# Performance work log

Measured on AMD Instinct MI355X. Metric: run time of the kernel, lower is better.

Reference implementation:

```python
import jax, jax.numpy as jnp
import numpy as np

NEG_SLOPE = 0.01  # torch nn.LeakyReLU default


def setup_inputs() -> dict:
    key = jax.random.key(0)
    k1, k2, k3, k4 = jax.random.split(key, 4)
    B, N, d = 256, 64, 64
    embeddings = jax.random.normal(k1, (B, N, d), dtype=jnp.float32)
    # nn.Linear(em_dim, em_dim): weight [d, d] (out, in), bias [d]
    w_W = jax.random.normal(k2, (d, d), dtype=jnp.float32) / np.sqrt(d)
    w_b = jax.random.normal(k3, (d,), dtype=jnp.float32) * 0.01
    # nn.Linear(em_dim, 1): weight [1, d] -> stored as [d], bias [1]
    a_W = jax.random.normal(k4, (d,), dtype=jnp.float32) / np.sqrt(d)
    a_b = jnp.zeros((1,), dtype=jnp.float32)
    return {"embeddings": embeddings, "w_W": w_W, "w_b": w_b, "a_W": a_W, "a_b": a_b}


def reference(embeddings, w_W, w_b, a_W, a_b):
    # pairwise elementwise product: value[b,i,j,d] = emb[b,i,d] * emb[b,j,d]
    value = embeddings[:, :, None, :] * embeddings[:, None, :, :]  # [B,N,N,d]
    # small linear d->d (torch Linear: x @ W.T + b)
    qk = jnp.einsum('bijd,ed->bije', value, w_W) + w_b
    qk = jnp.where(qk >= 0, qk, NEG_SLOPE * qk)  # LeakyReLU
    # dropout is identity in eval mode
    logits = jnp.einsum('bijd,d->bij', qk, a_W) + a_b[0]  # linear d->1, squeeze
    alphas = jax.nn.softmax(logits, axis=-1)[..., None]  # [B,N,N,1]
    return alphas, value
```

## Files before the change

kernel.cpp:

```cpp
#include <hip/hip_runtime.h>

typedef __attribute__((ext_vector_type(8))) short short8;
typedef __attribute__((ext_vector_type(4))) float floatx4;
typedef __attribute__((ext_vector_type(4))) int   intx4;

#define NEG_SLOPE 0.01f

__device__ __forceinline__ short f2bf(float f) {
    unsigned u = __float_as_uint(f);
    unsigned r = (u + 0x7FFFu + ((u >> 16) & 1u)) >> 16;
    return (short)r;
}

__device__ __forceinline__ int pack2(float x, float y) {
    return (int)(unsigned short)f2bf(x) | ((int)(unsigned short)f2bf(y) << 16);
}

__global__ __launch_bounds__(256, 4)
void afm_kernel(const float* __restrict__ emb,
                const float* __restrict__ wW,
                const float* __restrict__ wb,
                const float* __restrict__ aW,
                float* __restrict__ aOut,
                float* __restrict__ vOut) {
    __shared__ __align__(16) char smem[29184];

    const int tid = threadIdx.x;
    const int blk = blockIdx.x;
    const int g   = blk >> 1;
    const int b   = g >> 4;
    const int iq  = g & 15;

    const float* embB = emb + (size_t)b * 4096;

    if ((blk & 1) == 0) {
        float (*sE)[64] = (float (*)[64])smem;
        #pragma unroll
        for (int k = 0; k < 4; ++k) {
            int f4 = k * 256 + tid;
            float4 x = *(const float4*)(embB + (f4 << 2));
            *(float4*)&sE[0][f4 << 2] = x;
        }
        __syncthreads();

        const int d0 = (tid & 15) << 2;
        const int jb = tid >> 4;
        floatx4 ei[4];
        #pragma unroll
        for (int il = 0; il < 4; ++il)
            ei[il] = *(floatx4*)&sE[iq * 4 + il][d0];

        #pragma unroll
        for (int c = 0; c < 16; ++c) {
            const int il = c >> 2;
            const int j  = ((c & 3) << 4) + jb;
            floatx4 ej = *(floatx4*)&sE[j][d0];
            floatx4 x  = ei[il] * ej;
            float* dst = vOut + ((size_t)(b * 64 + iq * 4 + il) << 12)
                              + ((c & 3) << 10) + (tid << 2);
            __builtin_nontemporal_store(x, (floatx4*)dst);
        }
        return;
    }

    float (*sW)[68]   = (float (*)[68])smem;
    short (*sEb)[72]  = (short (*)[72])(smem + 17408);
    float (*sei)[64]  = (float (*)[64])(smem + 26624);
    float *swb        = (float *)(smem + 27648);
    float *saw        = (float *)(smem + 27904);
    float (*slog)[64] = (float (*)[64])(smem + 28160);

    const int lane = tid & 63;
    const int w    = tid >> 6;
    const int i    = iq * 4 + w;

    {
        int row = tid >> 2;
        int c0  = (tid & 3) << 4;
        const float* src = embB + row * 64 + c0;
        float4 a0 = *(const float4*)(src);
        float4 a1 = *(const float4*)(src + 4);
        float4 a2 = *(const float4*)(src + 8);
        float4 a3 = *(const float4*)(src + 12);
        intx4 q0, q1;
        q0[0] = pack2(a0.x, a0.y); q0[1] = pack2(a0.z, a0.w);
        q0[2] = pack2(a1.x, a1.y); q0[3] = pack2(a1.z, a1.w);
        q1[0] = pack2(a2.x, a2.y); q1[1] = pack2(a2.z, a2.w);
        q1[2] = pack2(a3.x, a3.y); q1[3] = pack2(a3.z, a3.w);
        *(intx4*)&sEb[row][c0]     = q0;
        *(intx4*)&sEb[row][c0 + 8] = q1;

        const float* wsrc = wW + row * 64 + c0;
        float4 b0 = *(const float4*)(wsrc);
        float4 b1 = *(const float4*)(wsrc + 4);
        float4 b2 = *(const float4*)(wsrc + 8);
        float4 b3 = *(const float4*)(wsrc + 12);
        *(float4*)&sW[row][c0]      = b0;
        *(float4*)&sW[row][c0 + 4]  = b1;
        *(float4*)&sW[row][c0 + 8]  = b2;
        *(float4*)&sW[row][c0 + 12] = b3;

        sei[w][lane] = embB[i * 64 + lane];
        if (tid < 64)        swb[tid]       = wb[tid];
        else if (tid < 128)  saw[tid - 64]  = aW[tid - 64];
    }
    __syncthreads();

    const int lo = lane & 15, hi = lane >> 4;

    short8 bf[2][4];
    #pragma unroll
    for (int kt = 0; kt < 2; ++kt) {
        const int d0 = kt * 32 + hi * 8;
        float4 ei0 = *(float4*)&sei[w][d0];
        float4 ei1 = *(float4*)&sei[w][d0 + 4];
        #pragma unroll
        for (int et = 0; et < 4; ++et) {
            int e = et * 16 + lo;
            float4 w0 = *(float4*)&sW[e][d0];
            float4 w1 = *(float4*)&sW[e][d0 + 4];
            short8 t;
            t[0] = f2bf(w0.x * ei0.x); t[1] = f2bf(w0.y * ei0.y);
            t[2] = f2bf(w0.z * ei0.z); t[3] = f2bf(w0.w * ei0.w);
            t[4] = f2bf(w1.x * ei1.x); t[5] = f2bf(w1.y * ei1.y);
            t[6] = f2bf(w1.z * ei1.z); t[7] = f2bf(w1.w * ei1.w);
            bf[kt][et] = t;
        }
    }

    float wbv[4], awv[4];
    #pragma unroll
    for (int et = 0; et < 4; ++et) {
        int e = et * 16 + lo;
        wbv[et] = swb[e];
        awv[et] = saw[e];
    }

    float lg[16];
    #pragma unroll
    for (int jt = 0; jt < 4; ++jt) {
        floatx4 acc[4];
        #pragma unroll
        for (int et = 0; et < 4; ++et)
            acc[et] = (floatx4){0.f, 0.f, 0.f, 0.f};
        #pragma unroll
        for (int kt = 0; kt < 2; ++kt) {
            short8 af = *(short8*)&sEb[jt * 16 + lo][kt * 32 + hi * 8];
            #pragma unroll
            for (int et = 0; et < 4; ++et)
                acc[et] = __builtin_amdgcn_mfma_f32_16x16x32_bf16(
                    af, bf[kt][et], acc[et], 0, 0, 0);
        }
        #pragma unroll
        for (int r = 0; r < 4; ++r) {
            float p = 0.f;
            #pragma unroll
            for (int et = 0; et < 4; ++et) {
                float x = acc[et][r] + wbv[et];
                x = fmaxf(x, NEG_SLOPE * x);
                p += awv[et] * x;
            }
            p += __shfl_xor(p, 1);
            p += __shfl_xor(p, 2);
            p += __shfl_xor(p, 4);
            p += __shfl_xor(p, 8);
            lg[jt * 4 + r] = p;
        }
    }

    float m = lg[0];
    #pragma unroll
    for (int k = 1; k < 16; ++k) m = fmaxf(m, lg[k]);
    m = fmaxf(m, __shfl_xor(m, 16));
    m = fmaxf(m, __shfl_xor(m, 32));

    float ex[16];
    float s = 0.f;
    #pragma unroll
    for (int k = 0; k < 16; ++k) { ex[k] = __expf(lg[k] - m); s += ex[k]; }
    s += __shfl_xor(s, 16);
    s += __shfl_xor(s, 32);
    float inv = 1.f / s;

    if (lo == 0) {
        #pragma unroll
        for (int jt = 0; jt < 4; ++jt)
            #pragma unroll
            for (int r = 0; r < 4; ++r)
                slog[w][jt * 16 + hi * 4 + r] = ex[jt * 4 + r] * inv;
    }
    __syncthreads();
    aOut[((size_t)(b * 64 + i) << 6) + lane] = slog[w][lane];
}

extern "C" void kernel_launch(void* const* d_in, const int* in_sizes, int n_in,
                              void* d_out, int out_size, void* d_ws, size_t ws_size,
                              hipStream_t stream) {
    const float* emb = (const float*)d_in[0];
    const float* wW  = (const float*)d_in[1];
    const float* wb  = (const float*)d_in[2];
    const float* aW  = (const float*)d_in[3];
    float* aOut = (float*)d_out;
    float* vOut = aOut + (size_t)256 * 64 * 64;
    afm_kernel<<<8192, 256, 0, stream>>>(emb, wW, wb, aW, aOut, vOut);
}
```

Baseline: 289.4 us.

## Coarsen value-writer blocks to cover half a batch each

Value-product blocks are reduced from 4096 (each writing 4 rows of i) to 512, each covering 32 rows of i for one batch in a sequential loop, and these blocks are placed first in the grid. The embedding tile is loaded into shared memory once per half-batch instead of once per 4-row group, which cuts redundant global loads and block launch overhead. The risk is fewer, longer-running store blocks, which can reduce memory-level parallelism and cause tail imbalance on the dominant 256 MB write stream.

```diff
diff --git a/kernel.cpp b/kernel.cpp
--- a/kernel.cpp
+++ b/kernel.cpp
@@ -27,13 +27,12 @@
 
     const int tid = threadIdx.x;
     const int blk = blockIdx.x;
-    const int g   = blk >> 1;
-    const int b   = g >> 4;
-    const int iq  = g & 15;
-
-    const float* embB = emb + (size_t)b * 4096;
-
-    if ((blk & 1) == 0) {
+
+    if (blk < 512) {
+        const int b     = blk >> 1;
+        const int iBase = (blk & 1) << 5;
+        const float* embB = emb + (size_t)b * 4096;
+
         float (*sE)[64] = (float (*)[64])smem;
         #pragma unroll
         for (int k = 0; k < 4; ++k) {
@@ -43,25 +42,31 @@
         }
         __syncthreads();
 
-        const int d0 = (tid & 15) << 2;
-        const int jb = tid >> 4;
-        floatx4 ei[4];
-        #pragma unroll
-        for (int il = 0; il < 4; ++il)
-            ei[il] = *(floatx4*)&sE[iq * 4 + il][d0];
-
-        #pragma unroll
-        for (int c = 0; c < 16; ++c) {
-            const int il = c >> 2;
-            const int j  = ((c & 3) << 4) + jb;
-            floatx4 ej = *(floatx4*)&sE[j][d0];
-            floatx4 x  = ei[il] * ej;
-            float* dst = vOut + ((size_t)(b * 64 + iq * 4 + il) << 12)
-                              + ((c & 3) << 10) + (tid << 2);
-            __builtin_nontemporal_store(x, (floatx4*)dst);
+        const int lane = tid & 63;
+        const int w    = tid >> 6;
+        const int d0   = (lane & 15) << 2;
+        const int jo   = lane >> 4;
+
+        #pragma unroll 1
+        for (int s = 0; s < 8; ++s) {
+            const int i = iBase + (s << 2) + w;
+            floatx4 ei = *(floatx4*)&sE[i][d0];
+            float* slab = vOut + ((size_t)(b * 64 + i) << 12);
+            #pragma unroll
+            for (int c = 0; c < 16; ++c) {
+                floatx4 ej = *(floatx4*)&sE[(c << 2) + jo][d0];
+                floatx4 x  = ei * ej;
+                __builtin_nontemporal_store(
+                    x, (floatx4*)(slab + (c << 8) + (lane << 2)));
+            }
         }
         return;
     }
+
+    const int g  = blk - 512;
+    const int b  = g >> 4;
+    const int iq = g & 15;
+    const float* embB = emb + (size_t)b * 4096;
 
     float (*sW)[68]   = (float (*)[68])smem;
     short (*sEb)[72]  = (short (*)[72])(smem + 17408);
@@ -202,5 +207,5 @@
     const float* aW  = (const float*)d_in[3];
     float* aOut = (float*)d_out;
     float* vOut = aOut + (size_t)256 * 64 * 64;
-    afm_kernel<<<8192, 256, 0, stream>>>(emb, wW, wb, aW, aOut, vOut);
-}
+    afm_kernel<<<4608, 256, 0, stream>>>(emb, wW, wb, aW, aOut, vOut);
+}
```

New measurement: 299.9 us. 3.6% more time.
